# Kernel tuning notes

Measured on AMD Instinct MI355X. Metric: run time of the kernel, lower is better.

The kernel has to match this reference:

```python
import jax, jax.numpy as jnp
import numpy as np

EPS = 1e-5
NUM_CRYSTALS = 64


def _bn(x2d, g, b):
    # torch BatchNorm1d in training mode: biased batch stats, affine
    m = x2d.mean(0)
    v = x2d.var(0)
    return g * (x2d - m) * jax.lax.rsqrt(v + EPS) + b


def _improved_conv(x, e, idx, p):
    (fcW, fcb, g1, b1, g2, b2, eW, eb, ge, be, W3, b3, g3, b3b) = p
    N, M = idx.shape
    A = x.shape[1]
    Bf = e.shape[2]
    xn = x[idx]  # (N, M, A) gathered neighbor atom features
    tot = jnp.concatenate([jnp.broadcast_to(x[:, None, :], (N, M, A)), xn, e], axis=2)  # (N,M,2A+B)
    # 2-body gated message
    h = jnp.einsum('nmf,of->nmo', tot, fcW) + fcb
    h = _bn(h.reshape(-1, 2 * A), g1, b1).reshape(N, M, 2 * A)
    two_body = jnp.sum(jax.nn.sigmoid(h[..., :A]) * jax.nn.softplus(h[..., A:]), axis=1)
    # explicit edge update
    he = jnp.einsum('nmf,of->nmo', tot, eW) + eb
    he = _bn(he.reshape(-1, 2 * Bf), ge, be).reshape(N, M, 2 * Bf)
    e_out = e + jax.nn.sigmoid(he[..., :Bf]) * jax.nn.softplus(he[..., Bf:])
    # 3-body: split W3 by concat blocks [x_i, x_j, x_l, e_ij, e_il] so the
    # (N,M,M,3A+2B) concat is never materialized; only (N,M,M,2A) is formed.
    Wa, Wj, Wl, Wij, Wil = jnp.split(W3, [A, 2 * A, 3 * A, 3 * A + Bf], axis=1)
    h3 = ((x @ Wa.T)[:, None, None, :]
          + (xn @ Wj.T)[:, :, None, :]
          + (xn @ Wl.T)[:, None, :, :]
          + (e @ Wij.T)[:, :, None, :]
          + (e @ Wil.T)[:, None, :, :]
          + b3)  # (N, M, M, 2A)
    h3 = _bn(h3.reshape(-1, 2 * A), g3, b3b).reshape(N, M, M, 2 * A)
    three_body = jnp.sum(jax.nn.sigmoid(h3[..., :A]) * jax.nn.softplus(h3[..., A:]), axis=(1, 2))
    total = _bn(two_body + three_body, g2, b2)
    return jax.nn.softplus(x + total), e_out


def setup_inputs() -> dict:
    key = jax.random.key(0)
    ks = jax.random.split(key, 12)
    N, M, OF, A, BF, H, NC = 2000, 12, 92, 64, 41, 128, 3
    f = lambda k, s: jax.random.normal(k, s, dtype=jnp.float32) * 0.05
    z = lambda s: jnp.zeros(s, jnp.float32)
    o = lambda s: jnp.ones(s, jnp.float32)
    return {
        'atom_fea': jax.random.normal(ks[0], (N, OF), dtype=jnp.float32),
        'nbr_fea': jax.random.normal(ks[1], (N, M, BF), dtype=jnp.float32),
        'nbr_fea_idx': jax.random.randint(ks[2], (N, M), 0, N),
        'site_seg': jnp.sort(jax.random.randint(ks[3], (N,), 0, NUM_CRYSTALS)),
        'emb_W': f(ks[4], (A, OF)), 'emb_b': z((A,)),
        'fcW': f(ks[5], (NC, 2 * A, 2 * A + BF)), 'fcb': z((NC, 2 * A)),
        'bn1_g': o((NC, 2 * A)), 'bn1_b': z((NC, 2 * A)),
        'bn2_g': o((NC, A)), 'bn2_b': z((NC, A)),
        'eW': f(ks[6], (NC, 2 * BF, 2 * A + BF)), 'eb': z((NC, 2 * BF)),
        'bne_g': o((NC, 2 * BF)), 'bne_b': z((NC, 2 * BF)),
        'W3': f(ks[7], (NC, 2 * A, 3 * A + 2 * BF)), 'b3': z((NC, 2 * A)),
        'bn3_g': o((NC, 2 * A)), 'bn3_b': z((NC, 2 * A)),
        'fc1W': f(ks[8], (H, A)), 'fc1b': z((H,)),
        'outW': f(ks[9], (1, H)), 'outb': z((1,)),
    }


def reference(atom_fea, nbr_fea, nbr_fea_idx, site_seg, emb_W, emb_b,
              fcW, fcb, bn1_g, bn1_b, bn2_g, bn2_b, eW, eb, bne_g, bne_b,
              W3, b3, bn3_g, bn3_b, fc1W, fc1b, outW, outb):
    x = atom_fea @ emb_W.T + emb_b  # embedding1 (orbital=False)
    e = nbr_fea
    n_conv = fcW.shape[0]
    for i in range(n_conv):  # small fixed layer loop
        p = (fcW[i], fcb[i], bn1_g[i], bn1_b[i], bn2_g[i], bn2_b[i],
             eW[i], eb[i], bne_g[i], bne_b[i], W3[i], b3[i], bn3_g[i], bn3_b[i])
        x, e = _improved_conv(x, e, nbr_fea_idx, p)
    x = jax.nn.softplus(jax.nn.softplus(x) @ fc1W.T + fc1b)  # conv_to_fc1
    # per-crystal mean pooling over site segments
    N = x.shape[0]
    sums = jax.ops.segment_sum(x, site_seg, num_segments=NUM_CRYSTALS)
    counts = jax.ops.segment_sum(jnp.ones((N, 1), x.dtype), site_seg, num_segments=NUM_CRYSTALS)
    pooled = sums / jnp.maximum(counts, 1.0)
    return pooled @ outW.T + outb  # (NUM_CRYSTALS, 1)
```

## Files before the change

kernel.cpp:

```cpp
#include <hip/hip_runtime.h>
#include <hip/hip_bf16.h>

#define N_ATOM 2000
#define MNBR   12
#define OFEA   92
#define AF     64
#define BFEA   41
#define K1     169
#define O1     128
#define OE     82
#define K3     274
#define NM     24000
#define NCONV  3
#define HID    128
#define NCRY   64
#define EPS_BN 1e-5f

#define LDA_T  192
#define LDH    512
#define LDSW   88

typedef __bf16 bf16x8 __attribute__((ext_vector_type(8)));
typedef float  f32x4  __attribute__((ext_vector_type(4)));

__device__ __forceinline__ float sigmoidf_(float x){
    return __builtin_amdgcn_rcpf(1.f + __expf(-x));
}
__device__ __forceinline__ float softplusf_(float x){
    return fmaxf(x,0.f) + __logf(1.f + __expf(-fabsf(x)));
}

__global__ __launch_bounds__(256)
void gemm_bf16(const __hip_bfloat16* __restrict__ A,
               const __hip_bfloat16* __restrict__ W,
               const float* __restrict__ bias,
               float* __restrict__ C)
{
    __shared__ unsigned short As[128][LDSW];
    __shared__ unsigned short Ws[128][LDSW];
    const int tid  = threadIdx.x;
    const int row0 = blockIdx.x * 128;
    const int col0 = blockIdx.y * 128;
    const int w    = tid >> 6;
    const int l    = tid & 63;
    const int wm   = w >> 1, wn = w & 1;
    const int lrow = l & 15;
    const int quad = l >> 4;

    f32x4 acc[4][4];
    #pragma unroll
    for (int i=0;i<4;i++)
        #pragma unroll
        for (int j=0;j<4;j++) acc[i][j] = (f32x4){0.f,0.f,0.f,0.f};

    for (int it = 0; it < 3; ++it){
        const int k0 = it * 64;
        if (it) __syncthreads();
        #pragma unroll
        for (int j = 0; j < 4; ++j){
            int e  = tid + j*256;
            int r  = e >> 3;
            int kk = (e & 7) << 3;
            int grow = row0 + r;
            uint4 va = make_uint4(0,0,0,0);
            if (grow < NM)
                va = *(const uint4*)(A + (size_t)grow*LDA_T + k0 + kk);
            *(uint4*)(&As[r][kk]) = va;
            uint4 vw = *(const uint4*)(W + (size_t)(col0 + r)*LDA_T + k0 + kk);
            *(uint4*)(&Ws[r][kk]) = vw;
        }
        __syncthreads();
        #pragma unroll
        for (int ks = 0; ks < 2; ++ks){
            int koff = ks*32 + quad*8;
            bf16x8 a_[4], b_[4];
            #pragma unroll
            for (int mi=0;mi<4;mi++)
                a_[mi] = *(const bf16x8*)(&As[wm*64 + mi*16 + lrow][koff]);
            #pragma unroll
            for (int ni=0;ni<4;ni++)
                b_[ni] = *(const bf16x8*)(&Ws[wn*64 + ni*16 + lrow][koff]);
            #pragma unroll
            for (int mi=0;mi<4;mi++)
                #pragma unroll
                for (int ni=0;ni<4;ni++)
                    acc[mi][ni] = __builtin_amdgcn_mfma_f32_16x16x32_bf16(
                        a_[mi], b_[ni], acc[mi][ni], 0, 0, 0);
        }
    }
    #pragma unroll
    for (int ni=0;ni<4;ni++){
        int col = col0 + wn*64 + ni*16 + lrow;
        float bv = bias[col];
        #pragma unroll
        for (int mi=0;mi<4;mi++){
            int rbase = row0 + wm*64 + mi*16 + quad*4;
            #pragma unroll
            for (int reg=0;reg<4;reg++){
                int grow = rbase + reg;
                if (grow < NM)
                    C[(size_t)grow*LDH + col] = acc[mi][ni][reg] + bv;
            }
        }
    }
}

#define BM 64
#define BN 128
#define BK 32
template<int EPI, int SPIN>
__global__ __launch_bounds__(256)
void gemm_tn(const float* __restrict__ T, int ldt, int R,
             const float* __restrict__ W, int ldw, int K, int O,
             const float* __restrict__ bias,
             float* __restrict__ C, int ldc)
{
    __shared__ float Ts[BM][BK+1];
    __shared__ float Ws2[BN][BK+1];
    const int tid = threadIdx.x;
    const int row0 = blockIdx.x * BM;
    const int tx = tid % 16;
    const int ty = tid / 16;
    float acc[4][8];
    #pragma unroll
    for (int i=0;i<4;i++)
        #pragma unroll
        for (int j=0;j<8;j++) acc[i][j]=0.f;

    for (int k0 = 0; k0 < K; k0 += BK) {
        #pragma unroll
        for (int i=0;i<(BM*BK)/256;i++){
            int e = tid + i*256;
            int r = e / BK, k = e % BK;
            int gr = row0 + r, gk = k0 + k;
            float v = 0.f;
            if (gr < R && gk < K){
                v = T[(size_t)gr*ldt + gk];
                if (SPIN) v = softplusf_(v);
            }
            Ts[r][k] = v;
        }
        #pragma unroll
        for (int i=0;i<(BN*BK)/256;i++){
            int e = tid + i*256;
            int r = e / BK, k = e % BK;
            int gk = k0 + k;
            Ws2[r][k] = (r < O && gk < K) ? W[(size_t)r*ldw + gk] : 0.f;
        }
        __syncthreads();
        #pragma unroll
        for (int k=0;k<BK;k++){
            float a_[4], b_[8];
            #pragma unroll
            for (int i=0;i<4;i++) a_[i] = Ts[ty*4+i][k];
            #pragma unroll
            for (int j=0;j<8;j++) b_[j] = Ws2[tx + j*16][k];
            #pragma unroll
            for (int i=0;i<4;i++)
                #pragma unroll
                for (int j=0;j<8;j++)
                    acc[i][j] += a_[i]*b_[j];
        }
        __syncthreads();
    }
    #pragma unroll
    for (int i=0;i<4;i++){
        int gr = row0 + ty*4 + i;
        if (gr >= R) continue;
        #pragma unroll
        for (int j=0;j<8;j++){
            int gc = tx + j*16;
            if (gc >= O) continue;
            float v = acc[i][j] + (bias ? bias[gc] : 0.f);
            if (EPI==1) v = softplusf_(v);
            C[(size_t)gr*ldc + gc] = v;
        }
    }
}

__global__ void pack_all(const float* __restrict__ fcW, const float* __restrict__ eW,
                         const float* __restrict__ W3, const float* __restrict__ fcb,
                         const float* __restrict__ eb, const float* __restrict__ b3,
                         __hip_bfloat16* __restrict__ WALL, float* __restrict__ BIAS)
{
    int i = blockIdx.x*blockDim.x + threadIdx.x;
    const int nW = NCONV*512*LDA_T;
    if (i < nW){
        int l = i/(512*LDA_T), rem = i%(512*LDA_T);
        int c = rem/LDA_T, k = rem%LDA_T;
        float v = 0.f;
        if (c < O1){
            if (k < K1) v = fcW[((size_t)l*O1 + c)*K1 + k];
        } else if (c < O1+OE){
            if (k < K1) v = eW[((size_t)l*OE + (c-O1))*K1 + k];
        } else if (c >= 256 && c < 384){
            int o = c - 256;
            const float* W3l = W3 + (size_t)l*O1*K3;
            if (k < AF)                        v = 0.5f * W3l[(size_t)o*K3 + k];
            else if (k < 2*AF)                 v = W3l[(size_t)o*K3 + k];
            else if (k < K1)                   v = W3l[(size_t)o*K3 + 192 + (k-128)];
        } else if (c >= 384){
            int o = c - 384;
            const float* W3l = W3 + (size_t)l*O1*K3;
            if (k < AF)                        v = 0.5f * W3l[(size_t)o*K3 + k];
            else if (k < 2*AF)                 v = W3l[(size_t)o*K3 + k + AF];
            else if (k < K1)                   v = W3l[(size_t)o*K3 + 233 + (k-128)];
        }
        WALL[i] = __float2bfloat16(v);
    } else if (i < nW + NCONV*512){
        int m = i - nW;
        int l = m/512, c = m%512;
        float v = 0.f;
        if (c < O1)         v = fcb[l*O1 + c];
        else if (c < O1+OE) v = eb[l*OE + (c-O1)];
        else if (c >= 256)  v = 0.5f * b3[l*O1 + ((c-256)&127)];
        BIAS[m] = v;
    }
}

__global__ void gather_b(__hip_bfloat16* __restrict__ TOT, const float* __restrict__ X,
                         const float* __restrict__ E, const int* __restrict__ idx)
{
    int i = blockIdx.x*blockDim.x + threadIdx.x;
    if (i >= NM*24) return;
    int grp = i % 24, r = i / 24;
    int n = r / MNBR;
    float v[8];
    if (grp < 16){
        const float* src = (grp < 8) ? (X + (size_t)n*AF + grp*8)
                                     : (X + (size_t)idx[r]*AF + (grp-8)*8);
        #pragma unroll
        for (int j=0;j<8;j++) v[j] = src[j];
    } else {
        int base = (grp-16)*8;
        #pragma unroll
        for (int j=0;j<8;j++){
            int k = base + j;
            v[j] = (k < BFEA) ? E[(size_t)r*BFEA + k] : 0.f;
        }
    }
    __hip_bfloat16 o[8];
    #pragma unroll
    for (int j=0;j<8;j++) o[j] = __float2bfloat16(v[j]);
    *(uint4*)(TOT + (size_t)r*LDA_T + grp*8) = *(const uint4*)o;
}

__global__ __launch_bounds__(256)
void stats_all(const float* __restrict__ REST,
               float* __restrict__ S1A, float* __restrict__ S2A,
               float* __restrict__ S13, float* __restrict__ S23)
{
    const int tid = threadIdx.x;
    const int n0 = blockIdx.x * 4;
    const int r0 = n0 * MNBR;
    if (tid < O1+OE){
        float s1 = 0.f, s2 = 0.f;
        #pragma unroll 4
        for (int j = 0; j < 4*MNBR; ++j){
            float v = REST[(size_t)(r0+j)*LDH + tid];
            s1 += v; s2 += v*v;
        }
        atomicAdd(&S1A[tid], s1);
        atomicAdd(&S2A[tid], s2);
    }
    if (tid < O1){
        float s1 = 0.f, s2 = 0.f;
        for (int a = 0; a < 4; ++a){
            int n = n0 + a;
            float sp=0.f, spp=0.f, sq=0.f, sqq=0.f;
            #pragma unroll
            for (int m=0;m<MNBR;m++){
                const float* row = REST + (size_t)(n*MNBR+m)*LDH;
                float p = row[256 + tid];
                float q = row[384 + tid];
                sp += p; spp += p*p; sq += q; sqq += q*q;
            }
            s1 += 12.f*(sp+sq);
            s2 += 12.f*(spp+sqq) + 2.f*sp*sq;
        }
        atomicAdd(&S13[tid], s1);
        atomicAdd(&S23[tid], s2);
    }
}

__global__ void bn_fin_all(const float* __restrict__ S1A, const float* __restrict__ S2A,
                           const float* __restrict__ S13, const float* __restrict__ S23,
                           const float* __restrict__ g1, const float* __restrict__ b1,
                           const float* __restrict__ ge, const float* __restrict__ be,
                           const float* __restrict__ g3, const float* __restrict__ b3b,
                           float* __restrict__ SC)
{
    int c = threadIdx.x;
    if (c < O1+OE){
        float mean = S1A[c]*(1.f/NM);
        float var  = fmaxf(S2A[c]*(1.f/NM) - mean*mean, 0.f);
        float gg = (c < O1) ? g1[c] : ge[c-O1];
        float bb = (c < O1) ? b1[c] : be[c-O1];
        float sc = gg * rsqrtf(var + EPS_BN);
        SC[c] = sc; SC[256+c] = bb - sc*mean;
    }
    if (c < O1){
        float mean = S13[c]*(1.f/((float)NM*MNBR));
        float var  = fmaxf(S23[c]*(1.f/((float)NM*MNBR)) - mean*mean, 0.f);
        float sc = g3[c] * rsqrtf(var + EPS_BN);
        SC[512+c] = sc; SC[640+c] = b3b[c] - sc*mean;
    }
}

__global__ __launch_bounds__(128)
void consumer_k(const float* __restrict__ REST, const float* __restrict__ SC,
                float* __restrict__ TB, float* __restrict__ E)
{
    __shared__ float red[128];
    const int n = blockIdx.x;
    const int t = threadIdx.x;
    const int a = t & 63;
    const int g = t >> 6;
    const float* base = REST + (size_t)n*MNBR*LDH;

    float sha = SC[a],      tha = SC[256+a];
    float shb = SC[64+a],   thb = SC[256+64+a];
    float s3lo = SC[512+a], s3hi = SC[512+64+a];
    float t3lo = SC[640+a], t3hi = SC[640+64+a];

    float Qa[MNBR], Qb[MNBR];
    #pragma unroll
    for (int m=0;m<MNBR;m++){
        const float* row = base + (size_t)m*LDH;
        Qa[m] = s3lo*row[384+a];
        Qb[m] = s3hi*row[448+a];
    }
    float acc = 0.f;
    #pragma unroll
    for (int j=0;j<6;j++){
        const float* row = base + (size_t)(g*6+j)*LDH;
        acc += sigmoidf_(sha*row[a]+tha) * softplusf_(shb*row[64+a]+thb);
        float ua = s3lo*row[256+a] + t3lo;
        float ub = s3hi*row[320+a] + t3hi;
        #pragma unroll
        for (int l2=0;l2<MNBR;l2++)
            acc += sigmoidf_(ua + Qa[l2]) * softplusf_(ub + Qb[l2]);
    }
    red[t] = acc;
    __syncthreads();
    if (g == 0)
        TB[(size_t)n*AF + a] = red[a] + red[64+a];
    for (int idx = t; idx < MNBR*BFEA; idx += 128){
        int m = idx / BFEA, b = idx % BFEA;
        const float* row = base + (size_t)m*LDH;
        float u = SC[O1+b]*row[O1+b]   + SC[256+O1+b];
        float v = SC[169+b]*row[169+b] + SC[256+169+b];
        E[(size_t)n*MNBR*BFEA + idx] += sigmoidf_(u) * softplusf_(v);
    }
}

__global__ __launch_bounds__(64)
void tb_stats_k(const float* __restrict__ TB,
                float* __restrict__ S1, float* __restrict__ S2)
{
    int t = threadIdx.x;
    float s1 = 0.f, s2 = 0.f;
    for (int r = blockIdx.x; r < N_ATOM; r += gridDim.x){
        float v = TB[(size_t)r*AF + t];
        s1 += v; s2 += v*v;
    }
    atomicAdd(&S1[t], s1);
    atomicAdd(&S2[t], s2);
}

__global__ void x_update_k(float* __restrict__ X, const float* __restrict__ TB,
                           const float* __restrict__ S12, const float* __restrict__ S22,
                           const float* __restrict__ g2, const float* __restrict__ b2,
                           int total)
{
    int i = blockIdx.x*blockDim.x + threadIdx.x;
    if (i >= total) return;
    int a = i & (AF-1);
    float mean = S12[a]*(1.f/N_ATOM);
    float var  = fmaxf(S22[a]*(1.f/N_ATOM) - mean*mean, 0.f);
    float sc = g2[a]*rsqrtf(var + EPS_BN);
    X[i] = softplusf_(X[i] + sc*TB[i] + (b2[a] - sc*mean));
}

__global__ __launch_bounds__(128)
void pool_out_k(const float* __restrict__ Z, const int* __restrict__ seg,
                const float* __restrict__ outW, const float* __restrict__ outb,
                float* __restrict__ out)
{
    __shared__ float red[128];
    const int c = blockIdx.x;
    const int h = threadIdx.x;
    int l0, l1;
    {
        int l=0, r=N_ATOM;
        while (l<r){ int m=(l+r)>>1; if (seg[m] < c) l=m+1; else r=m; }
        l0 = l;
        l=l0; r=N_ATOM;
        while (l<r){ int m=(l+r)>>1; if (seg[m] < c+1) l=m+1; else r=m; }
        l1 = l;
    }
    float s = 0.f;
    for (int n = l0; n < l1; ++n) s += Z[(size_t)n*HID + h];
    float cnt = fmaxf((float)(l1-l0), 1.f);
    red[h] = (s/cnt) * outW[h];
    __syncthreads();
    for (int off=64; off>0; off>>=1){
        if (h < off) red[h] += red[h+off];
        __syncthreads();
    }
    if (h == 0) out[c] = red[0] + outb[0];
}

extern "C" void kernel_launch(void* const* d_in, const int* in_sizes, int n_in,
                              void* d_out, int out_size, void* d_ws, size_t ws_size,
                              hipStream_t stream)
{
    const float* atom_fea = (const float*)d_in[0];
    const float* nbr_fea  = (const float*)d_in[1];
    const int*   nbr_idx  = (const int*)d_in[2];
    const int*   site_seg = (const int*)d_in[3];
    const float* emb_W = (const float*)d_in[4];
    const float* emb_b = (const float*)d_in[5];
    const float* fcW   = (const float*)d_in[6];
    const float* fcb   = (const float*)d_in[7];
    const float* bn1_g = (const float*)d_in[8];
    const float* bn1_b = (const float*)d_in[9];
    const float* bn2_g = (const float*)d_in[10];
    const float* bn2_b = (const float*)d_in[11];
    const float* eW    = (const float*)d_in[12];
    const float* eb    = (const float*)d_in[13];
    const float* bne_g = (const float*)d_in[14];
    const float* bne_b = (const float*)d_in[15];
    const float* W3    = (const float*)d_in[16];
    const float* b3    = (const float*)d_in[17];
    const float* bn3_g = (const float*)d_in[18];
    const float* bn3_b = (const float*)d_in[19];
    const float* fc1W  = (const float*)d_in[20];
    const float* fc1b  = (const float*)d_in[21];
    const float* outW  = (const float*)d_in[22];
    const float* outb  = (const float*)d_in[23];

    float* ws   = (float*)d_ws;
    float* X    = ws;
    float* E    = ws + 128000;
    __hip_bfloat16* TOT = (__hip_bfloat16*)(ws + 1112000);
    float* REST = ws + 3416000;
    float* TB   = ws + 15704000;
    float* ST   = ws + 15832000;
    float* SC   = ws + 15838144;
    __hip_bfloat16* WALL = (__hip_bfloat16*)(ws + 15839168);
    float* BIAS = ws + 15986624;
    float* Z    = ws + 15988224;

    {
        int tot = NCONV*512*LDA_T + NCONV*512;
        pack_all<<<(tot+255)/256, 256, 0, stream>>>(fcW, eW, W3, fcb, eb, b3, WALL, BIAS);
    }
    hipMemsetAsync(ST, 0, NCONV*2048*sizeof(float), stream);
    gemm_tn<0,0><<<(N_ATOM+BM-1)/BM, 256, 0, stream>>>(atom_fea, OFEA, N_ATOM,
                                                       emb_W, OFEA, OFEA, AF, emb_b, X, AF);
    hipMemcpyAsync(E, nbr_fea, (size_t)NM*BFEA*sizeof(float),
                   hipMemcpyDeviceToDevice, stream);

    for (int i = 0; i < NCONV; i++){
        const float* g1 = bn1_g + i*O1, *b1 = bn1_b + i*O1;
        const float* g2 = bn2_g + i*AF, *b2 = bn2_b + i*AF;
        const float* ge = bne_g + i*OE, *be = bne_b + i*OE;
        const float* g3 = bn3_g + i*O1, *b3b = bn3_b + i*O1;
        float* STL = ST + i*2048;
        float *S1A=STL, *S2A=STL+256, *S13=STL+512, *S23=STL+640, *S12=STL+768, *S22=STL+832;

        gather_b<<<(NM*24+255)/256, 256, 0, stream>>>(TOT, X, E, nbr_idx);
        {
            dim3 g((NM+127)/128, 4);
            gemm_bf16<<<g, 256, 0, stream>>>(TOT, WALL + (size_t)i*512*LDA_T,
                                             BIAS + i*512, REST);
        }
        stats_all<<<N_ATOM/4, 256, 0, stream>>>(REST, S1A, S2A, S13, S23);
        bn_fin_all<<<1, 256, 0, stream>>>(S1A, S2A, S13, S23,
                                          g1, b1, ge, be, g3, b3b, SC);
        consumer_k<<<N_ATOM, 128, 0, stream>>>(REST, SC, TB, E);
        tb_stats_k<<<128, 64, 0, stream>>>(TB, S12, S22);
        x_update_k<<<(N_ATOM*AF+255)/256, 256, 0, stream>>>(X, TB, S12, S22, g2, b2,
                                                            N_ATOM*AF);
    }

    gemm_tn<1,1><<<(N_ATOM+BM-1)/BM, 256, 0, stream>>>(X, AF, N_ATOM, fc1W, AF, AF, HID,
                                                       fc1b, Z, HID);
    pool_out_k<<<NCRY, 128, 0, stream>>>(Z, site_seg, outW, outb, (float*)d_out);
}
```

Before: 421.5 us.

## Fuse neighbor gather and BN statistics into the bf16 GEMM

The gather/bf16-pack step now happens inside the GEMM's shared-memory load, so the separate TOT staging buffer and gather kernel are removed. Edge features are kept in a padded 48-wide fp32 layout so rows can be read with float4 loads. Batch-norm sums and per-atom P/Q sums are accumulated in the GEMM epilogue through shared and global atomics, replacing the stats_all pass over REST, and a small bn3_pre kernel finishes the cross term. This adds atomic traffic and a larger memset, and it skips writing unused REST columns.

```diff
diff --git a/kernel.cpp b/kernel.cpp
--- a/kernel.cpp
+++ b/kernel.cpp
@@ -19,6 +19,7 @@
 #define LDA_T  192
 #define LDH    512
 #define LDSW   88
+#define LDE    48
 
 typedef __bf16 bf16x8 __attribute__((ext_vector_type(8)));
 typedef float  f32x4  __attribute__((ext_vector_type(4)));
@@ -30,14 +31,30 @@
     return fmaxf(x,0.f) + __logf(1.f + __expf(-fabsf(x)));
 }
 
-__global__ __launch_bounds__(256)
-void gemm_bf16(const __hip_bfloat16* __restrict__ A,
-               const __hip_bfloat16* __restrict__ W,
-               const float* __restrict__ bias,
-               float* __restrict__ C)
+__device__ __forceinline__ uint4 pack_bf16_8(const float* v){
+    __hip_bfloat16 o[8];
+    #pragma unroll
+    for (int j=0;j<8;j++) o[j] = __float2bfloat16(v[j]);
+    return *(const uint4*)o;
+}
+
+__global__ __launch_bounds__(256, 3)
+void gemm_fused(const float* __restrict__ X,
+                const float* __restrict__ E48,
+                const int*   __restrict__ idx,
+                const __hip_bfloat16* __restrict__ W,
+                const float* __restrict__ bias,
+                float* __restrict__ REST,
+                float* __restrict__ STL,
+                float* __restrict__ SPA,
+                float* __restrict__ SQA)
 {
     __shared__ unsigned short As[128][LDSW];
     __shared__ unsigned short Ws[128][LDSW];
+    __shared__ float cs1[128];
+    __shared__ float cs2[128];
+    __shared__ float spa[12][128];
+
     const int tid  = threadIdx.x;
     const int row0 = blockIdx.x * 128;
     const int col0 = blockIdx.y * 128;
@@ -47,12 +64,16 @@
     const int lrow = l & 15;
     const int quad = l >> 4;
 
+    if (tid < 128){ cs1[tid] = 0.f; cs2[tid] = 0.f; }
+    for (int ii = tid; ii < 12*128; ii += 256) spa[ii>>7][ii&127] = 0.f;
+
     f32x4 acc[4][4];
     #pragma unroll
     for (int i=0;i<4;i++)
         #pragma unroll
         for (int j=0;j<4;j++) acc[i][j] = (f32x4){0.f,0.f,0.f,0.f};
 
+    #pragma unroll
     for (int it = 0; it < 3; ++it){
         const int k0 = it * 64;
         if (it) __syncthreads();
@@ -62,10 +83,29 @@
             int r  = e >> 3;
             int kk = (e & 7) << 3;
             int grow = row0 + r;
-            uint4 va = make_uint4(0,0,0,0);
-            if (grow < NM)
-                va = *(const uint4*)(A + (size_t)grow*LDA_T + k0 + kk);
-            *(uint4*)(&As[r][kk]) = va;
+            float v[8];
+            #pragma unroll
+            for (int q2=0;q2<8;q2++) v[q2] = 0.f;
+            if (grow < NM){
+                if (it == 2){
+                    if (kk < LDE){
+                        const float* s = E48 + (size_t)grow*LDE + kk;
+                        float4 a0 = *(const float4*)s;
+                        float4 a1 = *(const float4*)(s+4);
+                        v[0]=a0.x; v[1]=a0.y; v[2]=a0.z; v[3]=a0.w;
+                        v[4]=a1.x; v[5]=a1.y; v[6]=a1.z; v[7]=a1.w;
+                    }
+                } else {
+                    const float* s = (it == 0)
+                        ? X + (size_t)((unsigned)grow/12u)*AF + kk
+                        : X + (size_t)idx[grow]*AF + kk;
+                    float4 a0 = *(const float4*)s;
+                    float4 a1 = *(const float4*)(s+4);
+                    v[0]=a0.x; v[1]=a0.y; v[2]=a0.z; v[3]=a0.w;
+                    v[4]=a1.x; v[5]=a1.y; v[6]=a1.z; v[7]=a1.w;
+                }
+            }
+            *(uint4*)(&As[r][kk]) = pack_bf16_8(v);
             uint4 vw = *(const uint4*)(W + (size_t)(col0 + r)*LDA_T + k0 + kk);
             *(uint4*)(&Ws[r][kk]) = vw;
         }
@@ -88,21 +128,88 @@
                         a_[mi], b_[ni], acc[mi][ni], 0, 0, 0);
         }
     }
+
+    const bool isPQ = (col0 >= 256);
+    const int atomBase = (unsigned)row0 / 12u;
+    int rbase_[4], n0_[4], sp_[4];
+    #pragma unroll
+    for (int mi=0;mi<4;mi++){
+        rbase_[mi] = row0 + wm*64 + mi*16 + quad*4;
+        int n0 = (int)((unsigned)rbase_[mi] / 12u);
+        n0_[mi] = n0;
+        sp_[mi] = 12 - (rbase_[mi] - n0*12);
+    }
+
     #pragma unroll
     for (int ni=0;ni<4;ni++){
-        int col = col0 + wn*64 + ni*16 + lrow;
-        float bv = bias[col];
+        const int cl  = wn*64 + ni*16 + lrow;
+        const int col = col0 + cl;
+        const float bv = bias[col];
+        float s1 = 0.f, s2 = 0.f;
         #pragma unroll
         for (int mi=0;mi<4;mi++){
-            int rbase = row0 + wm*64 + mi*16 + quad*4;
+            const int rbase = rbase_[mi];
+            float run0 = 0.f, run1 = 0.f;
             #pragma unroll
             for (int reg=0;reg<4;reg++){
                 int grow = rbase + reg;
-                if (grow < NM)
-                    C[(size_t)grow*LDH + col] = acc[mi][ni][reg] + bv;
+                if (grow < NM){
+                    float vv = acc[mi][ni][reg] + bv;
+                    if (col0 != 128 || col < 210)
+                        REST[(size_t)grow*LDH + col] = vv;
+                    s1 += vv; s2 += vv*vv;
+                    if (isPQ){
+                        if (reg < sp_[mi]) run0 += vv; else run1 += vv;
+                    }
+                }
             }
-        }
-    }
+            if (isPQ){
+                if (run0 != 0.f) atomicAdd(&spa[n0_[mi]     - atomBase][cl], run0);
+                if (run1 != 0.f) atomicAdd(&spa[n0_[mi] + 1 - atomBase][cl], run1);
+            }
+        }
+        if (isPQ){
+            atomicAdd(&cs2[cl], s2);
+        } else {
+            atomicAdd(&cs1[cl], s1);
+            atomicAdd(&cs2[cl], s2);
+        }
+    }
+    __syncthreads();
+    if (!isPQ){
+        if (tid < 128){
+            atomicAdd(&STL[col0 + tid],       cs1[tid]);
+            atomicAdd(&STL[256 + col0 + tid], cs2[tid]);
+        }
+    } else {
+        if (tid < 128)
+            atomicAdd(&STL[(col0 == 256 ? 896 : 1024) + tid], cs2[tid]);
+        float* SPQd = (col0 == 256) ? SPA : SQA;
+        for (int ii = tid; ii < 12*128; ii += 256){
+            int ai = ii >> 7, c2 = ii & 127;
+            int na = atomBase + ai;
+            float val = spa[ai][c2];
+            if (val != 0.f && na < N_ATOM)
+                atomicAdd(&SPQd[(size_t)na*128 + c2], val);
+        }
+    }
+}
+
+__global__ __launch_bounds__(256)
+void bn3_pre(const float* __restrict__ SPA, const float* __restrict__ SQA,
+             float* __restrict__ STL)
+{
+    const int c    = threadIdx.x & 127;
+    const int half = threadIdx.x >> 7;
+    float s1 = 0.f, sx = 0.f;
+    for (int n = blockIdx.x*2 + half; n < N_ATOM; n += 64){
+        float p = SPA[(size_t)n*128 + c];
+        float q = SQA[(size_t)n*128 + c];
+        s1 += p + q;
+        sx += p * q;
+    }
+    atomicAdd(&STL[512 + c], 12.f*s1);
+    atomicAdd(&STL[640 + c], 2.f*sx);
 }
 
 #define BM 64
@@ -218,79 +325,27 @@
     }
 }
 
-__global__ void gather_b(__hip_bfloat16* __restrict__ TOT, const float* __restrict__ X,
-                         const float* __restrict__ E, const int* __restrict__ idx)
+__global__ void e_init(const float* __restrict__ nbr, float* __restrict__ E48)
 {
     int i = blockIdx.x*blockDim.x + threadIdx.x;
-    if (i >= NM*24) return;
-    int grp = i % 24, r = i / 24;
-    int n = r / MNBR;
-    float v[8];
-    if (grp < 16){
-        const float* src = (grp < 8) ? (X + (size_t)n*AF + grp*8)
-                                     : (X + (size_t)idx[r]*AF + (grp-8)*8);
-        #pragma unroll
-        for (int j=0;j<8;j++) v[j] = src[j];
-    } else {
-        int base = (grp-16)*8;
-        #pragma unroll
-        for (int j=0;j<8;j++){
-            int k = base + j;
-            v[j] = (k < BFEA) ? E[(size_t)r*BFEA + k] : 0.f;
-        }
-    }
-    __hip_bfloat16 o[8];
-    #pragma unroll
-    for (int j=0;j<8;j++) o[j] = __float2bfloat16(v[j]);
-    *(uint4*)(TOT + (size_t)r*LDA_T + grp*8) = *(const uint4*)o;
-}
-
-__global__ __launch_bounds__(256)
-void stats_all(const float* __restrict__ REST,
-               float* __restrict__ S1A, float* __restrict__ S2A,
-               float* __restrict__ S13, float* __restrict__ S23)
-{
-    const int tid = threadIdx.x;
-    const int n0 = blockIdx.x * 4;
-    const int r0 = n0 * MNBR;
-    if (tid < O1+OE){
-        float s1 = 0.f, s2 = 0.f;
-        #pragma unroll 4
-        for (int j = 0; j < 4*MNBR; ++j){
-            float v = REST[(size_t)(r0+j)*LDH + tid];
-            s1 += v; s2 += v*v;
-        }
-        atomicAdd(&S1A[tid], s1);
-        atomicAdd(&S2A[tid], s2);
-    }
-    if (tid < O1){
-        float s1 = 0.f, s2 = 0.f;
-        for (int a = 0; a < 4; ++a){
-            int n = n0 + a;
-            float sp=0.f, spp=0.f, sq=0.f, sqq=0.f;
-            #pragma unroll
-            for (int m=0;m<MNBR;m++){
-                const float* row = REST + (size_t)(n*MNBR+m)*LDH;
-                float p = row[256 + tid];
-                float q = row[384 + tid];
-                sp += p; spp += p*p; sq += q; sqq += q*q;
-            }
-            s1 += 12.f*(sp+sq);
-            s2 += 12.f*(spp+sqq) + 2.f*sp*sq;
-        }
-        atomicAdd(&S13[tid], s1);
-        atomicAdd(&S23[tid], s2);
-    }
-}
-
-__global__ void bn_fin_all(const float* __restrict__ S1A, const float* __restrict__ S2A,
-                           const float* __restrict__ S13, const float* __restrict__ S23,
+    if (i >= NM*LDE) return;
+    int r = i / LDE, k = i % LDE;
+    E48[i] = (k < BFEA) ? nbr[(size_t)r*BFEA + k] : 0.f;
+}
+
+__global__ void bn_fin_all(const float* __restrict__ STL,
                            const float* __restrict__ g1, const float* __restrict__ b1,
                            const float* __restrict__ ge, const float* __restrict__ be,
                            const float* __restrict__ g3, const float* __restrict__ b3b,
                            float* __restrict__ SC)
 {
     int c = threadIdx.x;
+    const float* S1A = STL;
+    const float* S2A = STL + 256;
+    const float* S13 = STL + 512;
+    const float* S23 = STL + 640;
+    const float* S2P = STL + 896;
+    const float* S2Q = STL + 1024;
     if (c < O1+OE){
         float mean = S1A[c]*(1.f/NM);
         float var  = fmaxf(S2A[c]*(1.f/NM) - mean*mean, 0.f);
@@ -300,8 +355,10 @@
         SC[c] = sc; SC[256+c] = bb - sc*mean;
     }
     if (c < O1){
-        float mean = S13[c]*(1.f/((float)NM*MNBR));
-        float var  = fmaxf(S23[c]*(1.f/((float)NM*MNBR)) - mean*mean, 0.f);
+        float inv  = 1.f/((float)NM*MNBR);
+        float mean = S13[c]*inv;
+        float ex2  = (S23[c] + 12.f*(S2P[c] + S2Q[c]))*inv;
+        float var  = fmaxf(ex2 - mean*mean, 0.f);
         float sc = g3[c] * rsqrtf(var + EPS_BN);
         SC[512+c] = sc; SC[640+c] = b3b[c] - sc*mean;
     }
@@ -309,7 +366,7 @@
 
 __global__ __launch_bounds__(128)
 void consumer_k(const float* __restrict__ REST, const float* __restrict__ SC,
-                float* __restrict__ TB, float* __restrict__ E)
+                float* __restrict__ TB, float* __restrict__ E48)
 {
     __shared__ float red[128];
     const int n = blockIdx.x;
@@ -350,7 +407,7 @@
         const float* row = base + (size_t)m*LDH;
         float u = SC[O1+b]*row[O1+b]   + SC[256+O1+b];
         float v = SC[169+b]*row[169+b] + SC[256+169+b];
-        E[(size_t)n*MNBR*BFEA + idx] += sigmoidf_(u) * softplusf_(v);
+        E48[((size_t)n*MNBR + m)*LDE + b] += sigmoidf_(u) * softplusf_(v);
     }
 }
 
@@ -442,25 +499,24 @@
 
     float* ws   = (float*)d_ws;
     float* X    = ws;
-    float* E    = ws + 128000;
-    __hip_bfloat16* TOT = (__hip_bfloat16*)(ws + 1112000);
-    float* REST = ws + 3416000;
-    float* TB   = ws + 15704000;
-    float* ST   = ws + 15832000;
-    float* SC   = ws + 15838144;
-    __hip_bfloat16* WALL = (__hip_bfloat16*)(ws + 15839168);
-    float* BIAS = ws + 15986624;
-    float* Z    = ws + 15988224;
+    float* E48  = ws + 128000;
+    float* REST = ws + 1280000;
+    float* TB   = ws + 13568000;
+    float* Z    = ws + 13696000;
+    float* ST   = ws + 13952000;
+    float* SC   = ws + 13958144;
+    float* SPQ  = ws + 13959168;
+    __hip_bfloat16* WALL = (__hip_bfloat16*)(ws + 15495168);
+    float* BIAS = ws + 15642624;
 
     {
         int tot = NCONV*512*LDA_T + NCONV*512;
         pack_all<<<(tot+255)/256, 256, 0, stream>>>(fcW, eW, W3, fcb, eb, b3, WALL, BIAS);
     }
-    hipMemsetAsync(ST, 0, NCONV*2048*sizeof(float), stream);
+    hipMemsetAsync(ST, 0, (size_t)(6144 + 1024 + 1536000) * sizeof(float), stream);
     gemm_tn<0,0><<<(N_ATOM+BM-1)/BM, 256, 0, stream>>>(atom_fea, OFEA, N_ATOM,
                                                        emb_W, OFEA, OFEA, AF, emb_b, X, AF);
-    hipMemcpyAsync(E, nbr_fea, (size_t)NM*BFEA*sizeof(float),
-                   hipMemcpyDeviceToDevice, stream);
+    e_init<<<(NM*LDE+255)/256, 256, 0, stream>>>(nbr_fea, E48);
 
     for (int i = 0; i < NCONV; i++){
         const float* g1 = bn1_g + i*O1, *b1 = bn1_b + i*O1;
@@ -468,18 +524,19 @@
         const float* ge = bne_g + i*OE, *be = bne_b + i*OE;
         const float* g3 = bn3_g + i*O1, *b3b = bn3_b + i*O1;
         float* STL = ST + i*2048;
-        float *S1A=STL, *S2A=STL+256, *S13=STL+512, *S23=STL+640, *S12=STL+768, *S22=STL+832;
-
-        gather_b<<<(NM*24+255)/256, 256, 0, stream>>>(TOT, X, E, nbr_idx);
+        float* SPA = SPQ + (size_t)i*512000;
+        float* SQA = SPA + 256000;
+        float *S12 = STL+768, *S22 = STL+832;
+
         {
             dim3 g((NM+127)/128, 4);
-            gemm_bf16<<<g, 256, 0, stream>>>(TOT, WALL + (size_t)i*512*LDA_T,
-                                             BIAS + i*512, REST);
-        }
-        stats_all<<<N_ATOM/4, 256, 0, stream>>>(REST, S1A, S2A, S13, S23);
-        bn_fin_all<<<1, 256, 0, stream>>>(S1A, S2A, S13, S23,
-                                          g1, b1, ge, be, g3, b3b, SC);
-        consumer_k<<<N_ATOM, 128, 0, stream>>>(REST, SC, TB, E);
+            gemm_fused<<<g, 256, 0, stream>>>(X, E48, nbr_idx,
+                                              WALL + (size_t)i*512*LDA_T,
+                                              BIAS + i*512, REST, STL, SPA, SQA);
+        }
+        bn3_pre<<<32, 256, 0, stream>>>(SPA, SQA, STL);
+        bn_fin_all<<<1, 256, 0, stream>>>(STL, g1, b1, ge, be, g3, b3b, SC);
+        consumer_k<<<N_ATOM, 128, 0, stream>>>(REST, SC, TB, E48);
         tb_stats_k<<<128, 64, 0, stream>>>(TB, S12, S22);
         x_update_k<<<(N_ATOM*AF+255)/256, 256, 0, stream>>>(X, TB, S12, S22, g2, b2,
                                                             N_ATOM*AF);
```

Result: faster. 405.3 us (-3.8%).
